# Kernel optimization log

Measured on AMD Instinct MI355X. Metric: run time of the kernel, lower is better.

The kernel has to match this reference:

```python
import jax, jax.numpy as jnp
import numpy as np

SQRT_2 = 1.414213
RT = 1.0  # Disk sets self.rt = 1.0
N_KPTS = 8192
M_KPTS = 8192
F_DIM = 256  # SuperPoint descriptor dim


def setup_inputs() -> dict:
    key = jax.random.key(0)
    k0, k1, k2, k3 = jax.random.split(key, 4)
    d0 = jax.random.normal(k0, (1, F_DIM, N_KPTS), dtype=jnp.float32)
    d1 = jax.random.normal(k1, (1, F_DIM, M_KPTS), dtype=jnp.float32)
    # distance_matrix assumes L2-normalized descriptors (normalize over F axis)
    d0 = d0 / jnp.linalg.norm(d0, axis=1, keepdims=True)
    d1 = d1 / jnp.linalg.norm(d1, axis=1, keepdims=True)
    kpts0 = jax.random.uniform(k2, (1, N_KPTS, 2), dtype=jnp.float32) * 480.0
    kpts1 = jax.random.uniform(k3, (1, M_KPTS, 2), dtype=jnp.float32) * 480.0
    return {"descriptors0": d0, "descriptors1": d1,
            "keypoints0": kpts0, "keypoints1": kpts1}


def _ratio_nn(dist):
    """Per-row nearest neighbor + Lowe ratio test. dist: [A, B].
    Returns (nn_idx [A] int32, pass_mask [A] bool)."""
    neg2, idx2 = jax.lax.top_k(-dist, 2)  # two smallest distances per row
    d1, d2 = -neg2[:, 0], -neg2[:, 1]
    return idx2[:, 0], (d1 / d2) < RT


def reference(descriptors0, descriptors1, keypoints0, keypoints1):
    fs0 = descriptors0[0].T  # [N, F]
    fs1 = descriptors1[0].T  # [M, F]
    # cosine -> L2-on-unit-sphere distance matrix, clamped as in the source
    dist = SQRT_2 * jnp.sqrt(jnp.clip(1.0 - fs0 @ fs1.T, 1e-6, None))  # [N, M]

    fwd_nn, fwd_ok = _ratio_nn(dist)    # [N]
    bck_nn, bck_ok = _ratio_nn(dist.T)  # [M]

    # mutual NN: (i, fwd_nn[i]) is kept iff the backward pass produced the
    # flipped pair (i, fwd_nn[i]) too -> same as counts==2 in the torch merge
    n = fs0.shape[0]
    mutual = fwd_ok & bck_ok[fwd_nn] & (bck_nn[fwd_nn] == jnp.arange(n))

    indices0 = jnp.where(mutual, fwd_nn, -1)[None, :].astype(jnp.int32)  # [1, N]
    mscores0 = jnp.where(indices0 > 0, 1, 0).astype(jnp.int32)           # [1, N]
    matches1 = jnp.full(keypoints1.shape[:-1], -1, dtype=jnp.int32)      # [1, M]
    mscores1 = jnp.zeros(keypoints1.shape[:-1], dtype=keypoints1.dtype)  # [1, M]
    return indices0, matches1, mscores0, mscores1
```

## Files before the change

### kernel.cpp

```cpp
#include <hip/hip_runtime.h>
#include <float.h>

#define NPTS 8192
#define MPTS 8192
#define FDIM 256

#define BM 128
#define BN 128
#define BK 32
#define TCT (MPTS / BN)
#define TRT (NPTS / BM)

typedef unsigned short ushort_t;
typedef unsigned int u32;
typedef __attribute__((ext_vector_type(8))) short short8;
typedef __attribute__((ext_vector_type(4))) float floatx4;

struct T2 { float s1, s2; int i1; };

__device__ __forceinline__ T2 t2_sent() { T2 a; a.s1 = -FLT_MAX; a.s2 = -FLT_MAX; a.i1 = 0; return a; }

__device__ __forceinline__ T2 t2_merge(T2 a, T2 b) {
    T2 r;
    r.s1 = fmaxf(a.s1, b.s1);
    r.i1 = (b.s1 > a.s1) ? b.i1 : a.i1;
    r.s2 = fmaxf(fminf(a.s1, b.s1), fmaxf(a.s2, b.s2));
    return r;
}
__device__ __forceinline__ T2 t2_make4(float v0, float v1, float v2, float v3,
                                       int i0, int i1_, int i2, int i3) {
    float lo01 = fminf(v0, v1), hi01 = fmaxf(v0, v1);
    float lo23 = fminf(v2, v3), hi23 = fmaxf(v2, v3);
    int a01 = (v1 > v0) ? i1_ : i0;
    int a23 = (v3 > v2) ? i3 : i2;
    T2 r;
    r.s1 = fmaxf(hi01, hi23);
    r.i1 = (hi23 > hi01) ? a23 : a01;
    r.s2 = fmaxf(fminf(hi01, hi23), fmaxf(lo01, lo23));
    return r;
}
__device__ __forceinline__ float4 t2_pack(T2 a) {
    return make_float4(a.s1, a.s2, __int_as_float(a.i1), 0.0f);
}
__device__ __forceinline__ T2 t2_unpack(float4 v) {
    T2 a; a.s1 = v.x; a.s2 = v.y; a.i1 = __float_as_int(v.z); return a;
}
__device__ __forceinline__ T2 t2_shfl_xor(T2 a, int m) {
    T2 r; r.s1 = __shfl_xor(a.s1, m); r.s2 = __shfl_xor(a.s2, m); r.i1 = __shfl_xor(a.i1, m);
    return r;
}

__device__ __forceinline__ float bf2f(ushort_t u) {
    union { u32 i; float f; } v; v.i = ((u32)u) << 16; return v.f;
}
__device__ __forceinline__ ushort_t f2bf_rtne(float x) {
    u32 u = __float_as_uint(x);
    u32 r = u + 0x7FFFu + ((u >> 16) & 1u);
    return (ushort_t)(r >> 16);
}

__global__ __launch_bounds__(256) void transpose_split(
    const float* __restrict__ s0, const float* __restrict__ s1,
    ushort_t* __restrict__ hi0, ushort_t* __restrict__ lo0,
    ushort_t* __restrict__ hi1, ushort_t* __restrict__ lo1)
{
    __shared__ ushort_t hiS[64][66];
    __shared__ ushort_t loS[64][66];
    const float* src = blockIdx.z ? s1 : s0;
    ushort_t* hiT = blockIdx.z ? hi1 : hi0;
    ushort_t* loT = blockIdx.z ? lo1 : lo0;
    const int t = threadIdx.x;
    const int n0 = blockIdx.x * 64, f0 = blockIdx.y * 64;
#pragma unroll
    for (int p = 0; p < 16; p++) {
        int fl = (t >> 6) + p * 4;
        int nl = t & 63;
        float x = src[(size_t)(f0 + fl) * NPTS + n0 + nl];
        ushort_t hb = f2bf_rtne(x);
        ushort_t lb = f2bf_rtne(x - bf2f(hb));
        hiS[nl][fl] = hb;
        loS[nl][fl] = lb;
    }
    __syncthreads();
#pragma unroll
    for (int p = 0; p < 8; p++) {
        int nl = (t >> 5) + p * 8;
        int fp = (t & 31) * 2;
        u32 hw = (u32)hiS[nl][fp] | ((u32)hiS[nl][fp + 1] << 16);
        u32 lw = (u32)loS[nl][fp] | ((u32)loS[nl][fp + 1] << 16);
        size_t o = (size_t)(n0 + nl) * FDIM + f0 + fp;
        *(u32*)&hiT[o] = hw;
        *(u32*)&loT[o] = lw;
    }
}

#define GLDS(g, l) __builtin_amdgcn_global_load_lds( \
    (const __attribute__((address_space(1))) void*)(g), \
    (__attribute__((address_space(3))) void*)(l), 16, 0, 0)

__global__ __launch_bounds__(256, 2) void gemm_top2(
    const ushort_t* __restrict__ hiA, const ushort_t* __restrict__ loA,
    const ushort_t* __restrict__ hiB, const ushort_t* __restrict__ loB,
    float4* __restrict__ rowPart, float4* __restrict__ colPart)
{
    __shared__ char smem[36864];
    ushort_t* Ah = (ushort_t*)smem;
    ushort_t* Bh = (ushort_t*)(smem + 8192);
    ushort_t* Al = (ushort_t*)(smem + 16384);
    ushort_t* Bl = (ushort_t*)(smem + 24576);
    float* scrS1 = (float*)smem;
    float* scrS2 = (float*)(smem + 8448);
    int*   scrI  = (int*)(smem + 16896);
    float4* redC = (float4*)(smem + 25600);

    const int t = threadIdx.x;
    const int lane = t & 63, lc = lane & 15, q = lane >> 4;
    const int w = t >> 6, wx = w & 1, wy = w >> 1;
    const int ctile = blockIdx.x, rtile = blockIdx.y;
    const int n0 = rtile * BM, m0 = ctile * BN;

    floatx4 acc[4][4];
#pragma unroll
    for (int i = 0; i < 4; i++)
#pragma unroll
        for (int j = 0; j < 4; j++) acc[i][j] = (floatx4)0.0f;

    const int srow = t >> 2;
    const int skoff = (((t & 3) ^ ((t >> 3) & 3))) * 8;
    const size_t sldsOff = (size_t)t * 8;
    const int fkoff = (q ^ ((lc >> 1) & 3)) * 8;

    for (int k0 = 0; k0 < FDIM; k0 += BK) {
        if (k0) __syncthreads();
        GLDS(hiA + (size_t)(n0 + srow) * FDIM + k0 + skoff, Ah + sldsOff);
        GLDS(hiA + (size_t)(n0 + srow + 64) * FDIM + k0 + skoff, Ah + 2048 + sldsOff);
        GLDS(hiB + (size_t)(m0 + srow) * FDIM + k0 + skoff, Bh + sldsOff);
        GLDS(hiB + (size_t)(m0 + srow + 64) * FDIM + k0 + skoff, Bh + 2048 + sldsOff);
        GLDS(loA + (size_t)(n0 + srow) * FDIM + k0 + skoff, Al + sldsOff);
        GLDS(loA + (size_t)(n0 + srow + 64) * FDIM + k0 + skoff, Al + 2048 + sldsOff);
        GLDS(loB + (size_t)(m0 + srow) * FDIM + k0 + skoff, Bl + sldsOff);
        GLDS(loB + (size_t)(m0 + srow + 64) * FDIM + k0 + skoff, Bl + 2048 + sldsOff);
        __syncthreads();

        short8 ah[4], bh[4], al[4], bl[4];
#pragma unroll
        for (int i = 0; i < 4; i++) {
            int r = (wy * 64 + i * 16 + lc) * BK;
            ah[i] = *(const short8*)&Ah[r + fkoff];
            al[i] = *(const short8*)&Al[r + fkoff];
        }
#pragma unroll
        for (int j = 0; j < 4; j++) {
            int r = (wx * 64 + j * 16 + lc) * BK;
            bh[j] = *(const short8*)&Bh[r + fkoff];
            bl[j] = *(const short8*)&Bl[r + fkoff];
        }
#pragma unroll
        for (int i = 0; i < 4; i++)
#pragma unroll
            for (int j = 0; j < 4; j++) {
                acc[i][j] = __builtin_amdgcn_mfma_f32_16x16x32_bf16(ah[i], bh[j], acc[i][j], 0, 0, 0);
                acc[i][j] = __builtin_amdgcn_mfma_f32_16x16x32_bf16(ah[i], bl[j], acc[i][j], 0, 0, 0);
                acc[i][j] = __builtin_amdgcn_mfma_f32_16x16x32_bf16(al[i], bh[j], acc[i][j], 0, 0, 0);
            }
    }

    T2 colT[4];
#pragma unroll
    for (int j = 0; j < 4; j++) colT[j] = t2_sent();
    T2 rowT[4][4];

    const int cb = m0 + wx * 64 + lc;
#pragma unroll
    for (int i = 0; i < 4; i++) {
#pragma unroll
        for (int r = 0; r < 4; r++)
            rowT[i][r] = t2_make4(acc[i][0][r], acc[i][1][r], acc[i][2][r], acc[i][3][r],
                                  cb, cb + 16, cb + 32, cb + 48);
        const int rb = n0 + wy * 64 + i * 16 + q * 4;
#pragma unroll
        for (int j = 0; j < 4; j++)
            colT[j] = t2_merge(colT[j],
                t2_make4(acc[i][j][0], acc[i][j][1], acc[i][j][2], acc[i][j][3],
                         rb, rb + 1, rb + 2, rb + 3));
    }

#pragma unroll
    for (int j = 0; j < 4; j++) {
        colT[j] = t2_merge(colT[j], t2_shfl_xor(colT[j], 16));
        colT[j] = t2_merge(colT[j], t2_shfl_xor(colT[j], 32));
        if (q == 0) redC[(wx * 64 + j * 16 + lc) * 2 + wy] = t2_pack(colT[j]);
    }

#pragma unroll
    for (int round = 0; round < 2; round++) {
        __syncthreads();
        if (wy == round) {
#pragma unroll
            for (int i = 0; i < 4; i++)
#pragma unroll
                for (int r = 0; r < 4; r++) {
                    int row = i * 16 + q * 4 + r;
                    int col = (lc << 1) | wx;
                    int slot = row * 33 + ((col + row + 9 * q) & 31);
                    scrS1[slot] = rowT[i][r].s1;
                    scrS2[slot] = rowT[i][r].s2;
                    scrI[slot]  = rowT[i][r].i1;
                }
        }
        __syncthreads();
        {
            int row = t >> 2, chunk = t & 3;
            T2 a = t2_sent();
#pragma unroll
            for (int s = 0; s < 8; s++) {
                int slot = row * 33 + ((chunk << 3) | s);
                T2 b; b.s1 = scrS1[slot]; b.s2 = scrS2[slot]; b.i1 = scrI[slot];
                a = t2_merge(a, b);
            }
            a = t2_merge(a, t2_shfl_xor(a, 1));
            a = t2_merge(a, t2_shfl_xor(a, 2));
            if (chunk == 0)
                rowPart[(size_t)ctile * NPTS + n0 + round * 64 + row] = t2_pack(a);
        }
    }

    __syncthreads();
    if (t < 128) {
        T2 m = t2_unpack(redC[t * 2 + 0]);
        m = t2_merge(m, t2_unpack(redC[t * 2 + 1]));
        colPart[(size_t)rtile * MPTS + m0 + t] = t2_pack(m);
    }
}

__global__ __launch_bounds__(256) void reduce_cols(
    const float4* __restrict__ colPart, int* __restrict__ bck_nn, int* __restrict__ bck_ok)
{
    __shared__ float4 sh[4][64];
    const int t = threadIdx.x, ml = t & 63, sub = t >> 6;
    const int m = blockIdx.x * 64 + ml;
    T2 a = t2_sent();
#pragma unroll
    for (int k = 0; k < 16; k++)
        a = t2_merge(a, t2_unpack(colPart[(size_t)(sub * 16 + k) * MPTS + m]));
    sh[sub][ml] = t2_pack(a);
    __syncthreads();
    if (t < 64) {
        T2 r = t2_unpack(sh[0][t]);
        r = t2_merge(r, t2_unpack(sh[1][t]));
        r = t2_merge(r, t2_unpack(sh[2][t]));
        r = t2_merge(r, t2_unpack(sh[3][t]));
        float c1 = fmaxf(1.0f - r.s1, 1e-6f), c2 = fmaxf(1.0f - r.s2, 1e-6f);
        float d1 = 1.414213f * sqrtf(c1), d2 = 1.414213f * sqrtf(c2);
        int mm = blockIdx.x * 64 + t;
        bck_nn[mm] = r.i1;
        bck_ok[mm] = ((d1 / d2) < 1.0f) ? 1 : 0;
    }
}

__global__ __launch_bounds__(256) void reduce_rows_final(
    const float4* __restrict__ rowPart,
    const int* __restrict__ bck_nn, const int* __restrict__ bck_ok,
    float* __restrict__ out)
{
    __shared__ float4 sh[4][64];
    const int t = threadIdx.x, nl = t & 63, sub = t >> 6;
    const int n = blockIdx.x * 64 + nl;
    T2 a = t2_sent();
#pragma unroll
    for (int k = 0; k < 16; k++)
        a = t2_merge(a, t2_unpack(rowPart[(size_t)(sub * 16 + k) * NPTS + n]));
    sh[sub][nl] = t2_pack(a);
    __syncthreads();
    if (t < 64) {
        T2 r = t2_unpack(sh[0][t]);
        r = t2_merge(r, t2_unpack(sh[1][t]));
        r = t2_merge(r, t2_unpack(sh[2][t]));
        r = t2_merge(r, t2_unpack(sh[3][t]));
        float c1 = fmaxf(1.0f - r.s1, 1e-6f), c2 = fmaxf(1.0f - r.s2, 1e-6f);
        float d1 = 1.414213f * sqrtf(c1), d2 = 1.414213f * sqrtf(c2);
        int fwd = r.i1;
        bool ok = (d1 / d2) < 1.0f;
        bool mutual = ok && (bck_ok[fwd] != 0) && (bck_nn[fwd] == (blockIdx.x * 64 + t));
        int idx0 = mutual ? fwd : -1;
        int nn = blockIdx.x * 64 + t;
        out[nn]             = (float)idx0;
        out[NPTS + nn]      = -1.0f;
        out[2 * NPTS + nn]  = (idx0 > 0) ? 1.0f : 0.0f;
        out[3 * NPTS + nn]  = 0.0f;
    }
}

extern "C" void kernel_launch(void* const* d_in, const int* in_sizes, int n_in,
                              void* d_out, int out_size, void* d_ws, size_t ws_size,
                              hipStream_t stream)
{
    const float* d0 = (const float*)d_in[0];
    const float* d1 = (const float*)d_in[1];

    char* ws = (char*)d_ws;
    const size_t matB = (size_t)NPTS * FDIM * sizeof(ushort_t);
    ushort_t* hiA = (ushort_t*)(ws);
    ushort_t* loA = (ushort_t*)(ws + matB);
    ushort_t* hiB = (ushort_t*)(ws + 2 * matB);
    ushort_t* loB = (ushort_t*)(ws + 3 * matB);
    char* p = ws + 4 * matB;
    const size_t rowBytes = (size_t)TCT * NPTS * sizeof(float4);
    const size_t colBytes = (size_t)TRT * MPTS * sizeof(float4);
    float4* rowPart = (float4*)p;
    float4* colPart = (float4*)(p + rowBytes);
    int*    bck_nn  = (int*)(p + rowBytes + colBytes);
    int*    bck_ok  = bck_nn + MPTS;

    dim3 gt(NPTS / 64, FDIM / 64, 2);
    transpose_split<<<gt, 256, 0, stream>>>(d0, d1, hiA, loA, hiB, loB);

    dim3 g1(TCT, TRT);
    gemm_top2<<<g1, 256, 0, stream>>>(hiA, loA, hiB, loB, rowPart, colPart);
    reduce_cols<<<MPTS / 64, 256, 0, stream>>>(colPart, bck_nn, bck_ok);
    reduce_rows_final<<<NPTS / 64, 256, 0, stream>>>(rowPart, bck_nn, bck_ok,
                                                     (float*)d_out);
}
```

Baseline: 183.2 us.

## Switch GEMM to 32x32x16 MFMA tiles and fuse column reduction into final pass

Replaces the 16x16x32 bf16 MFMA tiling with 32x32x16 MFMA tiles, which changes the fragment layout, the LDS swizzle offsets and the top-2 epilogue. The row epilogue now runs in four per-wave rounds. Shared memory shrinks and the launch bound asks for three blocks per CU to raise occupancy. The two reduction kernels are merged into one that reduces only the column partials at each row's forward match, which skips the full backward reduction pass and one launch. The cost is gather-style reads of colPart and more LDS synchronization rounds in the epilogue.

Result: slower. 243.6 us (+33.0%).

```diff
diff --git a/kernel.cpp b/kernel.cpp
--- a/kernel.cpp
+++ b/kernel.cpp
@@ -14,7 +14,7 @@
 typedef unsigned short ushort_t;
 typedef unsigned int u32;
 typedef __attribute__((ext_vector_type(8))) short short8;
-typedef __attribute__((ext_vector_type(4))) float floatx4;
+typedef __attribute__((ext_vector_type(16))) float floatx16;
 
 struct T2 { float s1, s2; int i1; };
 
@@ -25,6 +25,12 @@
     r.s1 = fmaxf(a.s1, b.s1);
     r.i1 = (b.s1 > a.s1) ? b.i1 : a.i1;
     r.s2 = fmaxf(fminf(a.s1, b.s1), fmaxf(a.s2, b.s2));
+    return r;
+}
+__device__ __forceinline__ T2 t2_of2(float v0, int i0, float v1, int i1_) {
+    T2 r;
+    r.s1 = fmaxf(v0, v1); r.s2 = fminf(v0, v1);
+    r.i1 = (v1 > v0) ? i1_ : i0;
     return r;
 }
 __device__ __forceinline__ T2 t2_make4(float v0, float v1, float v2, float v3,
@@ -98,12 +104,12 @@
     (const __attribute__((address_space(1))) void*)(g), \
     (__attribute__((address_space(3))) void*)(l), 16, 0, 0)
 
-__global__ __launch_bounds__(256, 2) void gemm_top2(
+__global__ __launch_bounds__(256, 3) void gemm_top2(
     const ushort_t* __restrict__ hiA, const ushort_t* __restrict__ loA,
     const ushort_t* __restrict__ hiB, const ushort_t* __restrict__ loB,
     float4* __restrict__ rowPart, float4* __restrict__ colPart)
 {
-    __shared__ char smem[36864];
+    __shared__ char smem[32768];
     ushort_t* Ah = (ushort_t*)smem;
     ushort_t* Bh = (ushort_t*)(smem + 8192);
     ushort_t* Al = (ushort_t*)(smem + 16384);
@@ -114,21 +120,34 @@
     float4* redC = (float4*)(smem + 25600);
 
     const int t = threadIdx.x;
-    const int lane = t & 63, lc = lane & 15, q = lane >> 4;
+    const int lane = t & 63, cl = lane & 31, h = lane >> 5;
     const int w = t >> 6, wx = w & 1, wy = w >> 1;
     const int ctile = blockIdx.x, rtile = blockIdx.y;
     const int n0 = rtile * BM, m0 = ctile * BN;
 
-    floatx4 acc[4][4];
-#pragma unroll
-    for (int i = 0; i < 4; i++)
-#pragma unroll
-        for (int j = 0; j < 4; j++) acc[i][j] = (floatx4)0.0f;
+    floatx16 acc[2][2];
+#pragma unroll
+    for (int ti = 0; ti < 2; ti++)
+#pragma unroll
+        for (int tj = 0; tj < 2; tj++) acc[ti][tj] = (floatx16)0.0f;
 
     const int srow = t >> 2;
     const int skoff = (((t & 3) ^ ((t >> 3) & 3))) * 8;
     const size_t sldsOff = (size_t)t * 8;
-    const int fkoff = (q ^ ((lc >> 1) & 3)) * 8;
+
+    int aoff[2][2], boff[2][2];
+#pragma unroll
+    for (int ti = 0; ti < 2; ti++) {
+        int ra = wy * 64 + ti * 32 + cl, sw = (ra >> 1) & 3;
+#pragma unroll
+        for (int s = 0; s < 2; s++) aoff[ti][s] = ra * BK + ((s * 2 + h) ^ sw) * 8;
+    }
+#pragma unroll
+    for (int tj = 0; tj < 2; tj++) {
+        int rb = wx * 64 + tj * 32 + cl, sw = (rb >> 1) & 3;
+#pragma unroll
+        for (int s = 0; s < 2; s++) boff[tj][s] = rb * BK + ((s * 2 + h) ^ sw) * 8;
+    }
 
     for (int k0 = 0; k0 < FDIM; k0 += BK) {
         if (k0) __syncthreads();
@@ -142,86 +161,86 @@
         GLDS(loB + (size_t)(m0 + srow + 64) * FDIM + k0 + skoff, Bl + 2048 + sldsOff);
         __syncthreads();
 
-        short8 ah[4], bh[4], al[4], bl[4];
-#pragma unroll
-        for (int i = 0; i < 4; i++) {
-            int r = (wy * 64 + i * 16 + lc) * BK;
-            ah[i] = *(const short8*)&Ah[r + fkoff];
-            al[i] = *(const short8*)&Al[r + fkoff];
-        }
-#pragma unroll
-        for (int j = 0; j < 4; j++) {
-            int r = (wx * 64 + j * 16 + lc) * BK;
-            bh[j] = *(const short8*)&Bh[r + fkoff];
-            bl[j] = *(const short8*)&Bl[r + fkoff];
-        }
-#pragma unroll
-        for (int i = 0; i < 4; i++)
-#pragma unroll
-            for (int j = 0; j < 4; j++) {
-                acc[i][j] = __builtin_amdgcn_mfma_f32_16x16x32_bf16(ah[i], bh[j], acc[i][j], 0, 0, 0);
-                acc[i][j] = __builtin_amdgcn_mfma_f32_16x16x32_bf16(ah[i], bl[j], acc[i][j], 0, 0, 0);
-                acc[i][j] = __builtin_amdgcn_mfma_f32_16x16x32_bf16(al[i], bh[j], acc[i][j], 0, 0, 0);
+        short8 ah[2][2], al[2][2], bh[2][2], bl[2][2];
+#pragma unroll
+        for (int ti = 0; ti < 2; ti++)
+#pragma unroll
+            for (int s = 0; s < 2; s++) {
+                ah[ti][s] = *(const short8*)&Ah[aoff[ti][s]];
+                al[ti][s] = *(const short8*)&Al[aoff[ti][s]];
             }
-    }
-
-    T2 colT[4];
-#pragma unroll
-    for (int j = 0; j < 4; j++) colT[j] = t2_sent();
-    T2 rowT[4][4];
-
-    const int cb = m0 + wx * 64 + lc;
-#pragma unroll
-    for (int i = 0; i < 4; i++) {
-#pragma unroll
-        for (int r = 0; r < 4; r++)
-            rowT[i][r] = t2_make4(acc[i][0][r], acc[i][1][r], acc[i][2][r], acc[i][3][r],
-                                  cb, cb + 16, cb + 32, cb + 48);
-        const int rb = n0 + wy * 64 + i * 16 + q * 4;
-#pragma unroll
-        for (int j = 0; j < 4; j++)
-            colT[j] = t2_merge(colT[j],
-                t2_make4(acc[i][j][0], acc[i][j][1], acc[i][j][2], acc[i][j][3],
-                         rb, rb + 1, rb + 2, rb + 3));
-    }
-
-#pragma unroll
-    for (int j = 0; j < 4; j++) {
-        colT[j] = t2_merge(colT[j], t2_shfl_xor(colT[j], 16));
-        colT[j] = t2_merge(colT[j], t2_shfl_xor(colT[j], 32));
-        if (q == 0) redC[(wx * 64 + j * 16 + lc) * 2 + wy] = t2_pack(colT[j]);
-    }
-
-#pragma unroll
-    for (int round = 0; round < 2; round++) {
+#pragma unroll
+        for (int tj = 0; tj < 2; tj++)
+#pragma unroll
+            for (int s = 0; s < 2; s++) {
+                bh[tj][s] = *(const short8*)&Bh[boff[tj][s]];
+                bl[tj][s] = *(const short8*)&Bl[boff[tj][s]];
+            }
+#pragma unroll
+        for (int ti = 0; ti < 2; ti++)
+#pragma unroll
+            for (int tj = 0; tj < 2; tj++)
+#pragma unroll
+                for (int s = 0; s < 2; s++) {
+                    acc[ti][tj] = __builtin_amdgcn_mfma_f32_32x32x16_bf16(
+                        ah[ti][s], bh[tj][s], acc[ti][tj], 0, 0, 0);
+                    acc[ti][tj] = __builtin_amdgcn_mfma_f32_32x32x16_bf16(
+                        ah[ti][s], bl[tj][s], acc[ti][tj], 0, 0, 0);
+                    acc[ti][tj] = __builtin_amdgcn_mfma_f32_32x32x16_bf16(
+                        al[ti][s], bh[tj][s], acc[ti][tj], 0, 0, 0);
+                }
+    }
+
+
+#pragma unroll
+    for (int tj = 0; tj < 2; tj++) {
+        T2 p = t2_sent();
+#pragma unroll
+        for (int ti = 0; ti < 2; ti++)
+#pragma unroll
+            for (int g = 0; g < 4; g++) {
+                int rbase = n0 + wy * 64 + ti * 32 + 4 * h + 8 * g;
+                p = t2_merge(p, t2_make4(acc[ti][tj][g * 4 + 0], acc[ti][tj][g * 4 + 1],
+                                         acc[ti][tj][g * 4 + 2], acc[ti][tj][g * 4 + 3],
+                                         rbase, rbase + 1, rbase + 2, rbase + 3));
+            }
+        p = t2_merge(p, t2_shfl_xor(p, 32));
+        if (h == 0) redC[(wx * 64 + tj * 32 + cl) * 2 + wy] = t2_pack(p);
+    }
+
+    const int cb0 = m0 + wx * 64 + cl, cb1 = cb0 + 32;
+    const int rr = t >> 2, chunk = t & 3;
+    T2 runT = t2_sent();
+#pragma unroll
+    for (int round = 0; round < 4; round++) {
         __syncthreads();
-        if (wy == round) {
-#pragma unroll
-            for (int i = 0; i < 4; i++)
-#pragma unroll
-                for (int r = 0; r < 4; r++) {
-                    int row = i * 16 + q * 4 + r;
-                    int col = (lc << 1) | wx;
-                    int slot = row * 33 + ((col + row + 9 * q) & 31);
-                    scrS1[slot] = rowT[i][r].s1;
-                    scrS2[slot] = rowT[i][r].s2;
-                    scrI[slot]  = rowT[i][r].i1;
-                }
+        if (w == round) {
+#pragma unroll
+            for (int ti = 0; ti < 2; ti++)
+#pragma unroll
+                for (int g = 0; g < 4; g++)
+#pragma unroll
+                    for (int r4 = 0; r4 < 4; r4++) {
+                        int rl = ti * 32 + 4 * h + 8 * g + r4;
+                        T2 p = t2_of2(acc[ti][0][g * 4 + r4], cb0,
+                                      acc[ti][1][g * 4 + r4], cb1);
+                        int slot = rl * 33 + ((cl + rl) & 31);
+                        scrS1[slot] = p.s1; scrS2[slot] = p.s2; scrI[slot] = p.i1;
+                    }
         }
         __syncthreads();
-        {
-            int row = t >> 2, chunk = t & 3;
-            T2 a = t2_sent();
-#pragma unroll
-            for (int s = 0; s < 8; s++) {
-                int slot = row * 33 + ((chunk << 3) | s);
-                T2 b; b.s1 = scrS1[slot]; b.s2 = scrS2[slot]; b.i1 = scrI[slot];
-                a = t2_merge(a, b);
-            }
-            a = t2_merge(a, t2_shfl_xor(a, 1));
-            a = t2_merge(a, t2_shfl_xor(a, 2));
+#pragma unroll
+        for (int s2 = 0; s2 < 8; s2++) {
+            int slot = rr * 33 + (chunk * 8 + s2);
+            T2 b; b.s1 = scrS1[slot]; b.s2 = scrS2[slot]; b.i1 = scrI[slot];
+            runT = t2_merge(runT, b);
+        }
+        if (round & 1) {
+            runT = t2_merge(runT, t2_shfl_xor(runT, 1));
+            runT = t2_merge(runT, t2_shfl_xor(runT, 2));
             if (chunk == 0)
-                rowPart[(size_t)ctile * NPTS + n0 + round * 64 + row] = t2_pack(a);
+                rowPart[(size_t)ctile * NPTS + n0 + (round >> 1) * 64 + rr] = t2_pack(runT);
+            runT = t2_sent();
         }
     }
 
@@ -233,17 +252,21 @@
     }
 }
 
-__global__ __launch_bounds__(256) void reduce_cols(
-    const float4* __restrict__ colPart, int* __restrict__ bck_nn, int* __restrict__ bck_ok)
+__global__ __launch_bounds__(256) void reduce_final(
+    const float4* __restrict__ rowPart, const float4* __restrict__ colPart,
+    float* __restrict__ out)
 {
     __shared__ float4 sh[4][64];
-    const int t = threadIdx.x, ml = t & 63, sub = t >> 6;
-    const int m = blockIdx.x * 64 + ml;
+    __shared__ int shFwd[64];
+    __shared__ int shOk[64];
+    const int t = threadIdx.x, nl = t & 63, sub = t >> 6;
+    const int n = blockIdx.x * 64 + nl;
+
     T2 a = t2_sent();
 #pragma unroll
     for (int k = 0; k < 16; k++)
-        a = t2_merge(a, t2_unpack(colPart[(size_t)(sub * 16 + k) * MPTS + m]));
-    sh[sub][ml] = t2_pack(a);
+        a = t2_merge(a, t2_unpack(rowPart[(size_t)(sub * 16 + k) * NPTS + n]));
+    sh[sub][nl] = t2_pack(a);
     __syncthreads();
     if (t < 64) {
         T2 r = t2_unpack(sh[0][t]);
@@ -252,25 +275,16 @@
         r = t2_merge(r, t2_unpack(sh[3][t]));
         float c1 = fmaxf(1.0f - r.s1, 1e-6f), c2 = fmaxf(1.0f - r.s2, 1e-6f);
         float d1 = 1.414213f * sqrtf(c1), d2 = 1.414213f * sqrtf(c2);
-        int mm = blockIdx.x * 64 + t;
-        bck_nn[mm] = r.i1;
-        bck_ok[mm] = ((d1 / d2) < 1.0f) ? 1 : 0;
-    }
-}
-
-__global__ __launch_bounds__(256) void reduce_rows_final(
-    const float4* __restrict__ rowPart,
-    const int* __restrict__ bck_nn, const int* __restrict__ bck_ok,
-    float* __restrict__ out)
-{
-    __shared__ float4 sh[4][64];
-    const int t = threadIdx.x, nl = t & 63, sub = t >> 6;
-    const int n = blockIdx.x * 64 + nl;
-    T2 a = t2_sent();
+        shFwd[t] = r.i1;
+        shOk[t]  = ((d1 / d2) < 1.0f) ? 1 : 0;
+    }
+    __syncthreads();
+    const int fw = shFwd[nl];
+    T2 c = t2_sent();
 #pragma unroll
     for (int k = 0; k < 16; k++)
-        a = t2_merge(a, t2_unpack(rowPart[(size_t)(sub * 16 + k) * NPTS + n]));
-    sh[sub][nl] = t2_pack(a);
+        c = t2_merge(c, t2_unpack(colPart[(size_t)(sub * 16 + k) * MPTS + fw]));
+    sh[sub][nl] = t2_pack(c);
     __syncthreads();
     if (t < 64) {
         T2 r = t2_unpack(sh[0][t]);
@@ -279,11 +293,10 @@
         r = t2_merge(r, t2_unpack(sh[3][t]));
         float c1 = fmaxf(1.0f - r.s1, 1e-6f), c2 = fmaxf(1.0f - r.s2, 1e-6f);
         float d1 = 1.414213f * sqrtf(c1), d2 = 1.414213f * sqrtf(c2);
-        int fwd = r.i1;
-        bool ok = (d1 / d2) < 1.0f;
-        bool mutual = ok && (bck_ok[fwd] != 0) && (bck_nn[fwd] == (blockIdx.x * 64 + t));
-        int idx0 = mutual ? fwd : -1;
+        bool bok = (d1 / d2) < 1.0f;
         int nn = blockIdx.x * 64 + t;
+        bool mutual = (shOk[t] != 0) && bok && (r.i1 == nn);
+        int idx0 = mutual ? shFwd[t] : -1;
         out[nn]             = (float)idx0;
         out[NPTS + nn]      = -1.0f;
         out[2 * NPTS + nn]  = (idx0 > 0) ? 1.0f : 0.0f;
@@ -306,18 +319,13 @@
     ushort_t* loB = (ushort_t*)(ws + 3 * matB);
     char* p = ws + 4 * matB;
     const size_t rowBytes = (size_t)TCT * NPTS * sizeof(float4);
-    const size_t colBytes = (size_t)TRT * MPTS * sizeof(float4);
     float4* rowPart = (float4*)p;
     float4* colPart = (float4*)(p + rowBytes);
-    int*    bck_nn  = (int*)(p + rowBytes + colBytes);
-    int*    bck_ok  = bck_nn + MPTS;
 
     dim3 gt(NPTS / 64, FDIM / 64, 2);
     transpose_split<<<gt, 256, 0, stream>>>(d0, d1, hiA, loA, hiB, loB);
 
     dim3 g1(TCT, TRT);
     gemm_top2<<<g1, 256, 0, stream>>>(hiA, loA, hiB, loB, rowPart, colPart);
-    reduce_cols<<<MPTS / 64, 256, 0, stream>>>(colPart, bck_nn, bck_ok);
-    reduce_rows_final<<<NPTS / 64, 256, 0, stream>>>(rowPart, bck_nn, bck_ok,
-                                                     (float*)d_out);
-}
+    reduce_final<<<NPTS / 64, 256, 0, stream>>>(rowPart, colPart, (float*)d_out);
+}
```
